# Kernel tuning notes

Hardware: AMD Instinct MI355X
Metric: run time of the kernel (lower is better)

The kernel has to match this reference:

```python
import jax, jax.numpy as jnp
import numpy as np

B, N_GENES, N_SETS, G = 256, 10000, 1000, 128   # batch, input_dim, output_dim, geneset_size
H1, H2 = 64, 32                                  # hidden_dims
EPS = 1e-5                                       # BatchNorm1d eps


def _batchnorm(h, gamma, beta):
    # BatchNorm1d in training mode: biased batch stats over the batch axis
    mean = jnp.mean(h, axis=0, keepdims=True)
    var = jnp.mean(jnp.square(h - mean), axis=0, keepdims=True)
    return (h - mean) * jax.lax.rsqrt(var + EPS) * gamma + beta


def setup_inputs() -> dict:
    key = jax.random.key(0)
    ks = jax.random.split(key, 7)
    # Adjacency with exactly G distinct ones per column -> gather index list [N_SETS, G]
    rng = np.random.default_rng(0)
    gene_idx = np.argsort(rng.random((N_SETS, N_GENES)), axis=1)[:, :G]
    gene_idx = jnp.asarray(np.sort(gene_idx, axis=1), dtype=jnp.int32)

    x = jax.random.normal(ks[0], (B, N_GENES), jnp.float32)
    s1, s2, s3 = 1.0 / np.sqrt(G), 1.0 / np.sqrt(H1), 1.0 / np.sqrt(H2)
    W1 = jax.random.uniform(ks[1], (N_SETS, G, H1), jnp.float32, -s1, s1)
    b1 = jax.random.uniform(ks[2], (N_SETS, H1), jnp.float32, -s1, s1)
    W2 = jax.random.uniform(ks[3], (N_SETS, H1, H2), jnp.float32, -s2, s2)
    b2 = jax.random.uniform(ks[4], (N_SETS, H2), jnp.float32, -s2, s2)
    W3 = jax.random.uniform(ks[5], (N_SETS, H2), jnp.float32, -s3, s3)
    b3 = jax.random.uniform(ks[6], (N_SETS,), jnp.float32, -s3, s3)
    g1 = jnp.ones((N_SETS, H1), jnp.float32)
    be1 = jnp.zeros((N_SETS, H1), jnp.float32)
    g2 = jnp.ones((N_SETS, H2), jnp.float32)
    be2 = jnp.zeros((N_SETS, H2), jnp.float32)
    return {"x": x, "gene_idx": gene_idx, "W1": W1, "b1": b1, "g1": g1, "be1": be1,
            "W2": W2, "b2": b2, "g2": g2, "be2": be2, "W3": W3, "b3": b3}


def reference(x, gene_idx, W1, b1, g1, be1, W2, b2, g2, be2, W3, b3):
    # Per-geneset gather: x[:, adj[:,i]==1] for all i at once -> [B, S, G]
    xg = x[:, gene_idx]
    # Linear -> ReLU -> BatchNorm (per geneset, grouped GEMM)
    h = jax.nn.relu(jnp.einsum('bsg,sgh->bsh', xg, W1) + b1)
    h = _batchnorm(h, g1, be1)
    h = jax.nn.relu(jnp.einsum('bsh,shk->bsk', h, W2) + b2)
    h = _batchnorm(h, g2, be2)
    # Final Linear(H2 -> 1) -> ReLU, concatenated over genesets -> [B, S]
    out = jax.nn.relu(jnp.einsum('bsh,sh->bs', h, W3) + b3)
    return out
```

## Files before the change

### kernel.cpp

```cpp
#include <hip/hip_runtime.h>
#include <stdint.h>

#define BB 256
#define NG 10000
#define NS 1000
#define GG 128
#define H1 64
#define H2 32
#define EPSV 1e-5f


typedef unsigned short ushortT;
typedef __attribute__((ext_vector_type(4))) short short4v;
typedef __attribute__((ext_vector_type(8))) short short8v;
typedef __attribute__((ext_vector_type(4))) float float4v;

__device__ __forceinline__ float bf2f(ushortT u) {
    union { uint32_t i; float f; } v; v.i = ((uint32_t)u) << 16; return v.f;
}
__device__ __forceinline__ ushortT f2bf(float f) {
    union { float f; uint32_t i; } v; v.f = f;
    uint32_t x = v.i;
    return (ushortT)((x + 0x7fffu + ((x >> 16) & 1u)) >> 16);
}
__device__ __forceinline__ uint32_t pack2(ushortT lo, ushortT hi) {
    return (uint32_t)lo | ((uint32_t)hi << 16);
}
__device__ __forceinline__ bool probe_f32(const void* g1) {
    return ((*(const uint32_t*)g1) & 0xFFFFu) == 0u;
}
__device__ __forceinline__ float loadf(const void* p, int i, bool isf) {
    return isf ? ((const float*)p)[i] : bf2f(((const ushortT*)p)[i]);
}
__device__ __forceinline__ ushortT loadbf(const void* p, size_t i, bool isf) {
    return isf ? f2bf(((const float*)p)[i]) : ((const ushortT*)p)[i];
}

__global__ __launch_bounds__(256) void k_transpose(const void* __restrict__ x,
                                                   ushortT* __restrict__ xT,
                                                   const void* __restrict__ g1p) {
    __shared__ ushortT tile[64][66];
    const bool isf = probe_f32(g1p);
    const int tx = threadIdx.x & 63;
    const int tz = threadIdx.x >> 6;
    const int j0 = blockIdx.x * 64;
    const int b0 = blockIdx.y * 64;
    const int j = j0 + tx;
#pragma unroll
    for (int k = 0; k < 16; ++k) {
        int bl = tz * 16 + k;
        ushortT v = 0;
        if (j < NG) v = loadbf(x, (size_t)(b0 + bl) * NG + j, isf);
        tile[bl][tx] = v;
    }
    __syncthreads();
#pragma unroll
    for (int k = 0; k < 16; ++k) {
        int jl = tz * 16 + k;
        int jw = j0 + jl;
        if (jw < NG) xT[jw * BB + b0 + tx] = tile[tx][jl];
    }
}

__global__ __launch_bounds__(256, 4) void k_main(
    const ushortT* __restrict__ xT, const int* __restrict__ gidx,
    const void* __restrict__ W1, const void* __restrict__ W2,
    const void* __restrict__ b1, const void* __restrict__ g1, const void* __restrict__ be1,
    const void* __restrict__ b2, const void* __restrict__ g2, const void* __restrict__ be2,
    const void* __restrict__ W3, const void* __restrict__ b3,
    void* __restrict__ out) {
    __shared__ ushortT xg[BB * 68];
    __shared__ ushortT w1s[64 * 36];

    char* xgc = (char*)xg;
    float* redf = (float*)w1s;
    ushortT* w2s = w1s;

    const bool isf = probe_f32(g1);
    const int s = blockIdx.x;
    const int t = threadIdx.x;
    const int w = t >> 6;
    const int lane = t & 63;
    const int l16 = lane & 15;
    const int quad = lane >> 4;
    const size_t base1 = (size_t)s * (GG * H1);
    const size_t base2 = (size_t)s * (H1 * H2);

#define HOLEF(r0, k) (*(float*)(xgc + ((r0) + ((k) >> 1)) * 136 + 128 + ((k) & 1) * 4))

    const int gl = t >> 2;
    const int ml = t & 3;
    const int gid0 = gidx[s * GG + gl];
    const int gid1 = gidx[s * GG + 64 + gl];

    const float* W1f = (const float*)W1 + base1;
    const ushortT* W1h = (const ushortT*)W1 + base1;

    uint4 w1A0, w1A1, w1B0, w1B1;
    if (isf) {
        w1A0 = *(const uint4*)(W1f + (size_t)(0 * 512 + 0 * 256 + t) * 4);
        w1A1 = *(const uint4*)(W1f + (size_t)(0 * 512 + 1 * 256 + t) * 4);
        w1B0 = *(const uint4*)(W1f + (size_t)(1 * 512 + 0 * 256 + t) * 4);
        w1B1 = *(const uint4*)(W1f + (size_t)(1 * 512 + 1 * 256 + t) * 4);
    } else {
        w1A0 = *(const uint4*)(W1h + (size_t)0 * 2048 + t * 8);
        w1B0 = *(const uint4*)(W1h + (size_t)1 * 2048 + t * 8);
    }

    float b1v[4];
#pragma unroll
    for (int nt = 0; nt < 4; ++nt) b1v[nt] = loadf(b1, s * H1 + nt * 16 + l16, isf);
    float g1v = 0.f, be1v = 0.f;
    if (t < 64) { g1v = loadf(g1, s * H1 + t, isf); be1v = loadf(be1, s * H1 + t, isf); }

    auto stageF = [&](uint4 vv, int rr) {
        union { uint32_t i; float f; } u;
        const int g = rr * 16 + (t >> 4);
        const int h0 = (t & 15) * 4;
        u.i = vv.x; w1s[(h0 + 0) * 36 + g] = f2bf(u.f);
        u.i = vv.y; w1s[(h0 + 1) * 36 + g] = f2bf(u.f);
        u.i = vv.z; w1s[(h0 + 2) * 36 + g] = f2bf(u.f);
        u.i = vv.w; w1s[(h0 + 3) * 36 + g] = f2bf(u.f);
    };
    auto stageU = [&](uint4 vv) {
        const int g = t >> 3;
        const int h0 = (t & 7) * 8;
        w1s[(h0 + 0) * 36 + g] = (ushortT)vv.x;
        w1s[(h0 + 1) * 36 + g] = (ushortT)(vv.x >> 16);
        w1s[(h0 + 2) * 36 + g] = (ushortT)vv.y;
        w1s[(h0 + 3) * 36 + g] = (ushortT)(vv.y >> 16);
        w1s[(h0 + 4) * 36 + g] = (ushortT)vv.z;
        w1s[(h0 + 5) * 36 + g] = (ushortT)(vv.z >> 16);
        w1s[(h0 + 6) * 36 + g] = (ushortT)vv.w;
        w1s[(h0 + 7) * 36 + g] = (ushortT)(vv.w >> 16);
    };

    float4v acc1[4][4];
#pragma unroll
    for (int mt = 0; mt < 4; ++mt)
#pragma unroll
        for (int nt = 0; nt < 4; ++nt) acc1[mt][nt] = (float4v){0.f, 0.f, 0.f, 0.f};

    auto mfmaChunk = [&](int kt) {
        short8v bfrag[4];
#pragma unroll
        for (int nt = 0; nt < 4; ++nt) {
            const int h = nt * 16 + l16;
            const int woff = h * 36 + quad * 8;
            short4v blo = *(const short4v*)(&w1s[woff]);
            short4v bhi = *(const short4v*)(&w1s[woff + 4]);
            bfrag[nt] = __builtin_shufflevector(blo, bhi, 0, 1, 2, 3, 4, 5, 6, 7);
        }
#pragma unroll
        for (int mt = 0; mt < 4; ++mt) {
            const int b = w * 64 + mt * 16 + l16;
            const ushortT* p = &xg[b * 68 + kt * 32 + quad * 8];
            short4v alo = *(const short4v*)(p);
            short4v ahi = *(const short4v*)(p + 4);
            short8v af = __builtin_shufflevector(alo, ahi, 0, 1, 2, 3, 4, 5, 6, 7);
#pragma unroll
            for (int nt = 0; nt < 4; ++nt)
                acc1[mt][nt] = __builtin_amdgcn_mfma_f32_16x16x32_bf16(af, bfrag[nt], acc1[mt][nt], 0, 0, 0);
        }
    };

#pragma unroll
    for (int c = 0; c < 2; ++c) {
        const int gid = c ? gid1 : gid0;
        const ushortT* xrow = xT + (size_t)gid * BB;
        uint4 gv[4];
#pragma unroll
        for (int i = 0; i < 4; ++i) gv[i] = *(const uint4*)(xrow + (ml + 4 * i) * 8);

        __syncthreads();

#pragma unroll
        for (int i = 0; i < 4; ++i) {
            const int b0 = (ml + 4 * i) * 8;
            xg[(b0 + 0) * 68 + gl] = (ushortT)gv[i].x;
            xg[(b0 + 1) * 68 + gl] = (ushortT)(gv[i].x >> 16);
            xg[(b0 + 2) * 68 + gl] = (ushortT)gv[i].y;
            xg[(b0 + 3) * 68 + gl] = (ushortT)(gv[i].y >> 16);
            xg[(b0 + 4) * 68 + gl] = (ushortT)gv[i].z;
            xg[(b0 + 5) * 68 + gl] = (ushortT)(gv[i].z >> 16);
            xg[(b0 + 6) * 68 + gl] = (ushortT)gv[i].w;
            xg[(b0 + 7) * 68 + gl] = (ushortT)(gv[i].w >> 16);
        }
#pragma unroll
        for (int i = 0; i < 4; ++i) gv[i] = *(const uint4*)(xrow + (ml + 4 * i + 16) * 8);
#pragma unroll
        for (int i = 0; i < 4; ++i) {
            const int b0 = (ml + 4 * i + 16) * 8;
            xg[(b0 + 0) * 68 + gl] = (ushortT)gv[i].x;
            xg[(b0 + 1) * 68 + gl] = (ushortT)(gv[i].x >> 16);
            xg[(b0 + 2) * 68 + gl] = (ushortT)gv[i].y;
            xg[(b0 + 3) * 68 + gl] = (ushortT)(gv[i].y >> 16);
            xg[(b0 + 4) * 68 + gl] = (ushortT)gv[i].z;
            xg[(b0 + 5) * 68 + gl] = (ushortT)(gv[i].z >> 16);
            xg[(b0 + 6) * 68 + gl] = (ushortT)gv[i].w;
            xg[(b0 + 7) * 68 + gl] = (ushortT)(gv[i].w >> 16);
        }

        if (isf) { stageF(w1A0, 0); stageF(w1A1, 1); } else { stageU(w1A0); }
        if (c == 0) {
            if (isf) {
                w1A0 = *(const uint4*)(W1f + (size_t)(2 * 512 + 0 * 256 + t) * 4);
                w1A1 = *(const uint4*)(W1f + (size_t)(2 * 512 + 1 * 256 + t) * 4);
            } else {
                w1A0 = *(const uint4*)(W1h + (size_t)2 * 2048 + t * 8);
            }
        }
        __syncthreads();
        mfmaChunk(0);
        __syncthreads();
        if (isf) { stageF(w1B0, 0); stageF(w1B1, 1); } else { stageU(w1B0); }
        if (c == 0) {
            if (isf) {
                w1B0 = *(const uint4*)(W1f + (size_t)(3 * 512 + 0 * 256 + t) * 4);
                w1B1 = *(const uint4*)(W1f + (size_t)(3 * 512 + 1 * 256 + t) * 4);
            } else {
                w1B0 = *(const uint4*)(W1h + (size_t)3 * 2048 + t * 8);
            }
        }
        __syncthreads();
        mfmaChunk(1);
    }

    ushortT w2r[8];
    {
        const int k2 = t & 31, h0 = (t >> 5) * 8;
#pragma unroll
        for (int j = 0; j < 8; ++j) w2r[j] = loadbf(W2, base2 + (size_t)(h0 + j) * H2 + k2, isf);
    }
    float b2v[2], w3v[2];
#pragma unroll
    for (int nt = 0; nt < 2; ++nt) {
        b2v[nt] = loadf(b2, s * H2 + nt * 16 + l16, isf);
        w3v[nt] = loadf(W3, s * H2 + nt * 16 + l16, isf);
    }
    const float b3v = loadf(b3, s, isf);
    float g2v = 0.f, be2v = 0.f;
    if (t < 32) { g2v = loadf(g2, s * H2 + t, isf); be2v = loadf(be2, s * H2 + t, isf); }

    float s1v[4], s2v[4];
#pragma unroll
    for (int nt = 0; nt < 4; ++nt) {
        float s1 = 0.f, s2 = 0.f;
        const float bb = b1v[nt];
#pragma unroll
        for (int mt = 0; mt < 4; ++mt)
#pragma unroll
            for (int r = 0; r < 4; ++r) {
                float v = acc1[mt][nt][r] + bb;
                v = v > 0.f ? v : 0.f;
                s1 += v;
                s2 += v * v;
            }
        s1 += __shfl_xor(s1, 16); s1 += __shfl_xor(s1, 32);
        s2 += __shfl_xor(s2, 16); s2 += __shfl_xor(s2, 32);
        s1v[nt] = s1; s2v[nt] = s2;
    }
    __syncthreads();
    if (lane < 16) {
#pragma unroll
        for (int nt = 0; nt < 4; ++nt) {
            const int k = w * 64 + nt * 16 + lane;
            redf[k] = s1v[nt];
            redf[256 + k] = s2v[nt];
        }
    }
    __syncthreads();

    if (t < 64) {
        float ts = redf[t] + redf[64 + t] + redf[128 + t] + redf[192 + t];
        float tq = redf[256 + t] + redf[320 + t] + redf[384 + t] + redf[448 + t];
        float mean = ts * (1.0f / 256.0f);
        float var = tq * (1.0f / 256.0f) - mean * mean;
        var = var > 0.f ? var : 0.f;
        float rs = rsqrtf(var + EPSV);
        float a = g1v * rs;
        HOLEF(64, t) = a;
        HOLEF(96, t) = be1v - mean * a;
    }
    __syncthreads();

    {
        const int k2 = t & 31, h0 = (t >> 5) * 8;
        uint4 pk;
        pk.x = pack2(w2r[0], w2r[1]);
        pk.y = pack2(w2r[2], w2r[3]);
        pk.z = pack2(w2r[4], w2r[5]);
        pk.w = pack2(w2r[6], w2r[7]);
        *(uint4*)(&w2s[k2 * 72 + h0]) = pk;
    }
#pragma unroll
    for (int nt = 0; nt < 4; ++nt) {
        const int h = nt * 16 + l16;
        const float bb = b1v[nt];
        const float a = HOLEF(64, h), cc = HOLEF(96, h);
#pragma unroll
        for (int mt = 0; mt < 4; ++mt)
#pragma unroll
            for (int r = 0; r < 4; ++r) {
                const int b = w * 64 + mt * 16 + quad * 4 + r;
                float v = acc1[mt][nt][r] + bb;
                v = v > 0.f ? v : 0.f;
                xg[b * 68 + h] = f2bf(v * a + cc);
            }
    }
    __syncthreads();

    float4v acc2[4][2];
#pragma unroll
    for (int mt = 0; mt < 4; ++mt)
#pragma unroll
        for (int nt = 0; nt < 2; ++nt) acc2[mt][nt] = (float4v){0.f, 0.f, 0.f, 0.f};

#pragma unroll
    for (int kt = 0; kt < 2; ++kt) {
        const int kl = kt * 32 + quad * 8;
        short8v bfrag2[2];
#pragma unroll
        for (int nt = 0; nt < 2; ++nt) {
            const int k2 = nt * 16 + l16;
            const int woff = k2 * 72 + kl;
            short4v blo = *(const short4v*)(&w2s[woff]);
            short4v bhi = *(const short4v*)(&w2s[woff + 4]);
            bfrag2[nt] = __builtin_shufflevector(blo, bhi, 0, 1, 2, 3, 4, 5, 6, 7);
        }
#pragma unroll
        for (int mt = 0; mt < 4; ++mt) {
            const int b = w * 64 + mt * 16 + l16;
            const ushortT* p = &xg[b * 68 + kl];
            short4v alo = *(const short4v*)(p);
            short4v ahi = *(const short4v*)(p + 4);
            short8v af = __builtin_shufflevector(alo, ahi, 0, 1, 2, 3, 4, 5, 6, 7);
#pragma unroll
            for (int nt = 0; nt < 2; ++nt)
                acc2[mt][nt] = __builtin_amdgcn_mfma_f32_16x16x32_bf16(af, bfrag2[nt], acc2[mt][nt], 0, 0, 0);
        }
    }

#pragma unroll
    for (int nt = 0; nt < 2; ++nt) {
        float s1 = 0.f, s2 = 0.f;
        const float bb = b2v[nt];
#pragma unroll
        for (int mt = 0; mt < 4; ++mt)
#pragma unroll
            for (int r = 0; r < 4; ++r) {
                float v = acc2[mt][nt][r] + bb;
                v = v > 0.f ? v : 0.f;
                s1 += v;
                s2 += v * v;
            }
        s1 += __shfl_xor(s1, 16); s1 += __shfl_xor(s1, 32);
        s2 += __shfl_xor(s2, 16); s2 += __shfl_xor(s2, 32);
        if (lane < 16) {
            const int k = w * 32 + nt * 16 + lane;
            HOLEF(0, k) = s1;
            HOLEF(64, k) = s2;
        }
    }
    __syncthreads();

    if (t < 32) {
        float ts = HOLEF(0, t) + HOLEF(0, 32 + t) + HOLEF(0, 64 + t) + HOLEF(0, 96 + t);
        float tq = HOLEF(64, t) + HOLEF(64, 32 + t) + HOLEF(64, 64 + t) + HOLEF(64, 96 + t);
        float mean = ts * (1.0f / 256.0f);
        float var = tq * (1.0f / 256.0f) - mean * mean;
        var = var > 0.f ? var : 0.f;
        float rs = rsqrtf(var + EPSV);
        float a = g2v * rs;
        HOLEF(128, t) = a;
        HOLEF(144, t) = be2v - mean * a;
    }
    __syncthreads();

    float a2[2], c2[2];
#pragma unroll
    for (int nt = 0; nt < 2; ++nt) {
        const int k2 = nt * 16 + l16;
        a2[nt] = HOLEF(128, k2);
        c2[nt] = HOLEF(144, k2);
    }
#pragma unroll
    for (int mt = 0; mt < 4; ++mt)
#pragma unroll
        for (int r = 0; r < 4; ++r) {
            float tot = 0.f;
#pragma unroll
            for (int nt = 0; nt < 2; ++nt) {
                float v = acc2[mt][nt][r] + b2v[nt];
                v = v > 0.f ? v : 0.f;
                tot += (v * a2[nt] + c2[nt]) * w3v[nt];
            }
            tot += __shfl_xor(tot, 1);
            tot += __shfl_xor(tot, 2);
            tot += __shfl_xor(tot, 4);
            tot += __shfl_xor(tot, 8);
            if (l16 == 0) {
                const int b = w * 64 + mt * 16 + quad * 4 + r;
                float o = tot + b3v;
                o = o > 0.f ? o : 0.f;
                if (isf) ((float*)out)[b * NS + s] = o;
                else     ((ushortT*)out)[b * NS + s] = f2bf(o);
            }
        }
#undef HOLEF
}

extern "C" void kernel_launch(void* const* d_in, const int* in_sizes, int n_in,
                              void* d_out, int out_size, void* d_ws, size_t ws_size,
                              hipStream_t stream) {
    const int* gi = (const int*)d_in[1];
    ushortT* xT = (ushortT*)d_ws;

    dim3 gT((NG + 63) / 64, BB / 64);
    k_transpose<<<gT, 256, 0, stream>>>(d_in[0], xT, d_in[4]);
    k_main<<<NS, 256, 0, stream>>>(xT, gi, d_in[2], d_in[6],
                                   d_in[3], d_in[4], d_in[5],
                                   d_in[7], d_in[8], d_in[9], d_in[10], d_in[11],
                                   d_out);
}
```

Before: 134.2 us.

## Vectorize transpose, gather 4 genes per thread with perm packing, hardware bf16 converts

The transpose kernel now reads 4 elements per thread with vector loads and writes packed uint2 stores instead of scalar accesses. The main kernel gathers 4 gene rows per thread and interleaves them with byte permutes, so each LDS write is 64-bit instead of 16-bit. The W1 prefetch schedule is reordered around the two gather phases. Software float-to-bf16 rounding is replaced by the packed v_cvt_pk_bf16_f32 instruction, and the gidx load becomes a vector load; together these aim to cut instruction count and global/LDS transaction overhead. In exchange it relies on the inline asm being available on this target and raises register pressure from holding eight uint4 gather values.

```diff
diff --git a/kernel.cpp b/kernel.cpp
--- a/kernel.cpp
+++ b/kernel.cpp
@@ -23,6 +23,11 @@
     uint32_t x = v.i;
     return (ushortT)((x + 0x7fffu + ((x >> 16) & 1u)) >> 16);
 }
+__device__ __forceinline__ uint32_t cvtpk_bf16(float lo, float hi) {
+    uint32_t d;
+    asm("v_cvt_pk_bf16_f32 %0, %1, %2" : "=v"(d) : "v"(lo), "v"(hi));
+    return d;
+}
 __device__ __forceinline__ uint32_t pack2(ushortT lo, ushortT hi) {
     return (uint32_t)lo | ((uint32_t)hi << 16);
 }
@@ -41,24 +46,57 @@
                                                    const void* __restrict__ g1p) {
     __shared__ ushortT tile[64][66];
     const bool isf = probe_f32(g1p);
-    const int tx = threadIdx.x & 63;
-    const int tz = threadIdx.x >> 6;
+    const int q = threadIdx.x & 15;
+    const int r = threadIdx.x >> 4;
     const int j0 = blockIdx.x * 64;
     const int b0 = blockIdx.y * 64;
-    const int j = j0 + tx;
-#pragma unroll
-    for (int k = 0; k < 16; ++k) {
-        int bl = tz * 16 + k;
-        ushortT v = 0;
-        if (j < NG) v = loadbf(x, (size_t)(b0 + bl) * NG + j, isf);
-        tile[bl][tx] = v;
-    }
-    __syncthreads();
-#pragma unroll
-    for (int k = 0; k < 16; ++k) {
-        int jl = tz * 16 + k;
-        int jw = j0 + jl;
-        if (jw < NG) xT[jw * BB + b0 + tx] = tile[tx][jl];
+    const bool fullj = (j0 + 64 <= NG);
+#pragma unroll
+    for (int k = 0; k < 4; ++k) {
+        const int bl = k * 16 + r;
+        const int jq = q * 4;
+        const size_t src = (size_t)(b0 + bl) * NG + j0 + jq;
+        uint32_t d0, d1;
+        if (isf) {
+            if (fullj) {
+                float4 v = *(const float4*)((const float*)x + src);
+                d0 = cvtpk_bf16(v.x, v.y);
+                d1 = cvtpk_bf16(v.z, v.w);
+            } else {
+                float vx[4];
+#pragma unroll
+                for (int i2 = 0; i2 < 4; ++i2)
+                    vx[i2] = (j0 + jq + i2 < NG) ? ((const float*)x)[src + i2] : 0.f;
+                d0 = cvtpk_bf16(vx[0], vx[1]);
+                d1 = cvtpk_bf16(vx[2], vx[3]);
+            }
+        } else {
+            if (fullj) {
+                uint2 v = *(const uint2*)((const ushortT*)x + src);
+                d0 = v.x; d1 = v.y;
+            } else {
+                ushortT e[4];
+#pragma unroll
+                for (int i2 = 0; i2 < 4; ++i2)
+                    e[i2] = (j0 + jq + i2 < NG) ? ((const ushortT*)x)[src + i2] : (ushortT)0;
+                d0 = pack2(e[0], e[1]); d1 = pack2(e[2], e[3]);
+            }
+        }
+        *(uint32_t*)(&tile[bl][jq]) = d0;
+        *(uint32_t*)(&tile[bl][jq + 2]) = d1;
+    }
+    __syncthreads();
+#pragma unroll
+    for (int k = 0; k < 4; ++k) {
+        const int jl = k * 16 + r;
+        const int jw = j0 + jl;
+        if (jw < NG) {
+            const int bq = q * 4;
+            uint2 o;
+            o.x = pack2(tile[bq + 0][jl], tile[bq + 1][jl]);
+            o.y = pack2(tile[bq + 2][jl], tile[bq + 3][jl]);
+            *(uint2*)(&xT[(size_t)jw * BB + b0 + bq]) = o;
+        }
     }
 }
 
@@ -88,10 +126,10 @@
 
 #define HOLEF(r0, k) (*(float*)(xgc + ((r0) + ((k) >> 1)) * 136 + 128 + ((k) & 1) * 4))
 
-    const int gl = t >> 2;
-    const int ml = t & 3;
-    const int gid0 = gidx[s * GG + gl];
-    const int gid1 = gidx[s * GG + 64 + gl];
+    const int gq = t & 15;
+    const int bo2 = t >> 4;
+    const int B0 = bo2 * 16;
+    int4 gidA = *(const int4*)(gidx + s * GG + 4 * gq);
 
     const float* W1f = (const float*)W1 + base1;
     const ushortT* W1h = (const ushortT*)W1 + base1;
@@ -100,11 +138,8 @@
     if (isf) {
         w1A0 = *(const uint4*)(W1f + (size_t)(0 * 512 + 0 * 256 + t) * 4);
         w1A1 = *(const uint4*)(W1f + (size_t)(0 * 512 + 1 * 256 + t) * 4);
-        w1B0 = *(const uint4*)(W1f + (size_t)(1 * 512 + 0 * 256 + t) * 4);
-        w1B1 = *(const uint4*)(W1f + (size_t)(1 * 512 + 1 * 256 + t) * 4);
     } else {
         w1A0 = *(const uint4*)(W1h + (size_t)0 * 2048 + t * 8);
-        w1B0 = *(const uint4*)(W1h + (size_t)1 * 2048 + t * 8);
     }
 
     float b1v[4];
@@ -114,13 +149,16 @@
     if (t < 64) { g1v = loadf(g1, s * H1 + t, isf); be1v = loadf(be1, s * H1 + t, isf); }
 
     auto stageF = [&](uint4 vv, int rr) {
-        union { uint32_t i; float f; } u;
+        union { uint32_t i; float f; } u0, u1, u2, u3;
+        u0.i = vv.x; u1.i = vv.y; u2.i = vv.z; u3.i = vv.w;
         const int g = rr * 16 + (t >> 4);
         const int h0 = (t & 15) * 4;
-        u.i = vv.x; w1s[(h0 + 0) * 36 + g] = f2bf(u.f);
-        u.i = vv.y; w1s[(h0 + 1) * 36 + g] = f2bf(u.f);
-        u.i = vv.z; w1s[(h0 + 2) * 36 + g] = f2bf(u.f);
-        u.i = vv.w; w1s[(h0 + 3) * 36 + g] = f2bf(u.f);
+        const uint32_t p01 = cvtpk_bf16(u0.f, u1.f);
+        const uint32_t p23 = cvtpk_bf16(u2.f, u3.f);
+        w1s[(h0 + 0) * 36 + g] = (ushortT)p01;
+        w1s[(h0 + 1) * 36 + g] = (ushortT)(p01 >> 16);
+        w1s[(h0 + 2) * 36 + g] = (ushortT)p23;
+        w1s[(h0 + 3) * 36 + g] = (ushortT)(p23 >> 16);
     };
     auto stageU = [&](uint4 vv) {
         const int g = t >> 3;
@@ -141,6 +179,38 @@
 #pragma unroll
         for (int nt = 0; nt < 4; ++nt) acc1[mt][nt] = (float4v){0.f, 0.f, 0.f, 0.f};
 
+    uint4 gv[8];
+    auto gload = [&](const int4 g4) {
+        const ushortT* r0 = xT + (size_t)g4.x * BB + B0;
+        const ushortT* r1 = xT + (size_t)g4.y * BB + B0;
+        const ushortT* r2 = xT + (size_t)g4.z * BB + B0;
+        const ushortT* r3 = xT + (size_t)g4.w * BB + B0;
+        gv[0] = *(const uint4*)(r0); gv[1] = *(const uint4*)(r0 + 8);
+        gv[2] = *(const uint4*)(r1); gv[3] = *(const uint4*)(r1 + 8);
+        gv[4] = *(const uint4*)(r2); gv[5] = *(const uint4*)(r2 + 8);
+        gv[6] = *(const uint4*)(r3); gv[7] = *(const uint4*)(r3 + 8);
+    };
+    auto unpack = [&]() {
+#pragma unroll
+        for (int oc = 0; oc < 2; ++oc) {
+            const uint32_t aw[4] = {gv[0 + oc].x, gv[0 + oc].y, gv[0 + oc].z, gv[0 + oc].w};
+            const uint32_t bw[4] = {gv[2 + oc].x, gv[2 + oc].y, gv[2 + oc].z, gv[2 + oc].w};
+            const uint32_t cw[4] = {gv[4 + oc].x, gv[4 + oc].y, gv[4 + oc].z, gv[4 + oc].w};
+            const uint32_t dw[4] = {gv[6 + oc].x, gv[6 + oc].y, gv[6 + oc].z, gv[6 + oc].w};
+#pragma unroll
+            for (int p = 0; p < 4; ++p) {
+#pragma unroll
+                for (int hf = 0; hf < 2; ++hf) {
+                    const uint32_t sel = hf ? 0x07060302u : 0x05040100u;
+                    uint2 o;
+                    o.x = __builtin_amdgcn_perm(bw[p], aw[p], sel);
+                    o.y = __builtin_amdgcn_perm(dw[p], cw[p], sel);
+                    const int b = B0 + oc * 8 + p * 2 + hf;
+                    *(uint2*)(&xg[b * 68 + 4 * gq]) = o;
+                }
+            }
+        }
+    };
     auto mfmaChunk = [&](int kt) {
         short8v bfrag[4];
 #pragma unroll
@@ -164,67 +234,45 @@
         }
     };
 
-#pragma unroll
-    for (int c = 0; c < 2; ++c) {
-        const int gid = c ? gid1 : gid0;
-        const ushortT* xrow = xT + (size_t)gid * BB;
-        uint4 gv[4];
-#pragma unroll
-        for (int i = 0; i < 4; ++i) gv[i] = *(const uint4*)(xrow + (ml + 4 * i) * 8);
-
-        __syncthreads();
-
-#pragma unroll
-        for (int i = 0; i < 4; ++i) {
-            const int b0 = (ml + 4 * i) * 8;
-            xg[(b0 + 0) * 68 + gl] = (ushortT)gv[i].x;
-            xg[(b0 + 1) * 68 + gl] = (ushortT)(gv[i].x >> 16);
-            xg[(b0 + 2) * 68 + gl] = (ushortT)gv[i].y;
-            xg[(b0 + 3) * 68 + gl] = (ushortT)(gv[i].y >> 16);
-            xg[(b0 + 4) * 68 + gl] = (ushortT)gv[i].z;
-            xg[(b0 + 5) * 68 + gl] = (ushortT)(gv[i].z >> 16);
-            xg[(b0 + 6) * 68 + gl] = (ushortT)gv[i].w;
-            xg[(b0 + 7) * 68 + gl] = (ushortT)(gv[i].w >> 16);
-        }
-#pragma unroll
-        for (int i = 0; i < 4; ++i) gv[i] = *(const uint4*)(xrow + (ml + 4 * i + 16) * 8);
-#pragma unroll
-        for (int i = 0; i < 4; ++i) {
-            const int b0 = (ml + 4 * i + 16) * 8;
-            xg[(b0 + 0) * 68 + gl] = (ushortT)gv[i].x;
-            xg[(b0 + 1) * 68 + gl] = (ushortT)(gv[i].x >> 16);
-            xg[(b0 + 2) * 68 + gl] = (ushortT)gv[i].y;
-            xg[(b0 + 3) * 68 + gl] = (ushortT)(gv[i].y >> 16);
-            xg[(b0 + 4) * 68 + gl] = (ushortT)gv[i].z;
-            xg[(b0 + 5) * 68 + gl] = (ushortT)(gv[i].z >> 16);
-            xg[(b0 + 6) * 68 + gl] = (ushortT)gv[i].w;
-            xg[(b0 + 7) * 68 + gl] = (ushortT)(gv[i].w >> 16);
-        }
-
-        if (isf) { stageF(w1A0, 0); stageF(w1A1, 1); } else { stageU(w1A0); }
-        if (c == 0) {
-            if (isf) {
-                w1A0 = *(const uint4*)(W1f + (size_t)(2 * 512 + 0 * 256 + t) * 4);
-                w1A1 = *(const uint4*)(W1f + (size_t)(2 * 512 + 1 * 256 + t) * 4);
-            } else {
-                w1A0 = *(const uint4*)(W1h + (size_t)2 * 2048 + t * 8);
-            }
-        }
-        __syncthreads();
-        mfmaChunk(0);
-        __syncthreads();
-        if (isf) { stageF(w1B0, 0); stageF(w1B1, 1); } else { stageU(w1B0); }
-        if (c == 0) {
-            if (isf) {
-                w1B0 = *(const uint4*)(W1f + (size_t)(3 * 512 + 0 * 256 + t) * 4);
-                w1B1 = *(const uint4*)(W1f + (size_t)(3 * 512 + 1 * 256 + t) * 4);
-            } else {
-                w1B0 = *(const uint4*)(W1h + (size_t)3 * 2048 + t * 8);
-            }
-        }
-        __syncthreads();
-        mfmaChunk(1);
-    }
+    gload(gidA);
+    unpack();
+    int4 gidB = *(const int4*)(gidx + s * GG + 64 + 4 * gq);
+    if (isf) { stageF(w1A0, 0); stageF(w1A1, 1); } else { stageU(w1A0); }
+    if (isf) {
+        w1B0 = *(const uint4*)(W1f + (size_t)(1 * 512 + 0 * 256 + t) * 4);
+        w1B1 = *(const uint4*)(W1f + (size_t)(1 * 512 + 1 * 256 + t) * 4);
+    } else {
+        w1B0 = *(const uint4*)(W1h + (size_t)1 * 2048 + t * 8);
+    }
+    __syncthreads();
+    mfmaChunk(0);
+    __syncthreads();
+    if (isf) { stageF(w1B0, 0); stageF(w1B1, 1); } else { stageU(w1B0); }
+    if (isf) {
+        w1A0 = *(const uint4*)(W1f + (size_t)(2 * 512 + 0 * 256 + t) * 4);
+        w1A1 = *(const uint4*)(W1f + (size_t)(2 * 512 + 1 * 256 + t) * 4);
+    } else {
+        w1A0 = *(const uint4*)(W1h + (size_t)2 * 2048 + t * 8);
+    }
+    __syncthreads();
+    mfmaChunk(1);
+
+    gload(gidB);
+    __syncthreads();
+    unpack();
+    if (isf) { stageF(w1A0, 0); stageF(w1A1, 1); } else { stageU(w1A0); }
+    if (isf) {
+        w1B0 = *(const uint4*)(W1f + (size_t)(3 * 512 + 0 * 256 + t) * 4);
+        w1B1 = *(const uint4*)(W1f + (size_t)(3 * 512 + 1 * 256 + t) * 4);
+    } else {
+        w1B0 = *(const uint4*)(W1h + (size_t)3 * 2048 + t * 8);
+    }
+    __syncthreads();
+    mfmaChunk(0);
+    __syncthreads();
+    if (isf) { stageF(w1B0, 0); stageF(w1B1, 1); } else { stageU(w1B0); }
+    __syncthreads();
+    mfmaChunk(1);
 
     ushortT w2r[8];
     {
@@ -299,14 +347,17 @@
         const float bb = b1v[nt];
         const float a = HOLEF(64, h), cc = HOLEF(96, h);
 #pragma unroll
-        for (int mt = 0; mt < 4; ++mt)
-#pragma unroll
-            for (int r = 0; r < 4; ++r) {
-                const int b = w * 64 + mt * 16 + quad * 4 + r;
-                float v = acc1[mt][nt][r] + bb;
-                v = v > 0.f ? v : 0.f;
-                xg[b * 68 + h] = f2bf(v * a + cc);
-            }
+        for (int mt = 0; mt < 4; ++mt) {
+            const int b0r = w * 64 + mt * 16 + quad * 4;
+#pragma unroll
+            for (int rp = 0; rp < 2; ++rp) {
+                float v0 = acc1[mt][nt][2 * rp] + bb;     v0 = v0 > 0.f ? v0 : 0.f;
+                float v1 = acc1[mt][nt][2 * rp + 1] + bb; v1 = v1 > 0.f ? v1 : 0.f;
+                const uint32_t pk = cvtpk_bf16(v0 * a + cc, v1 * a + cc);
+                xg[(b0r + 2 * rp) * 68 + h] = (ushortT)pk;
+                xg[(b0r + 2 * rp + 1) * 68 + h] = (ushortT)(pk >> 16);
+            }
+        }
     }
     __syncthreads();
 
```

After: 134.1 us (median of 2 runs). No clear change (-0.1%).
